# Performance work log

Measured on AMD Instinct MI355X. Metric: run time of the kernel, lower is better.

## Reference

```python
import jax, jax.numpy as jnp
import numpy as np

P = 5.0  # p-norm order from init_kwargs


def setup_inputs() -> dict:
    key = jax.random.key(0)
    k1, k2 = jax.random.split(key)
    B, N, M, C = 8, 4096, 4096, 3
    x = jax.random.normal(k1, (B, N, C), dtype=jnp.float32)
    y = jax.random.normal(k2, (B, M, C), dtype=jnp.float32)
    return {"x": x, "y": y}


def _pnorm(v, axis):
    # (sum |v|^p)^(1/p), matching torch.norm(p=5)
    return jnp.sum(jnp.abs(v) ** P, axis=axis) ** (1.0 / P)


def reference(x, y):
    # Squared Euclidean distance matrix [B, N, M]
    d = (-2.0 * jnp.einsum("bnc,bmc->bnm", x, y)
         + jnp.sum(x * x, -1)[:, :, None]
         + jnp.sum(y * y, -1)[:, None, :])
    idx1 = jnp.argmin(d, axis=2)  # [B, N]: nearest y for each x
    idx2 = jnp.argmin(d, axis=1)  # [B, M]: nearest x for each y
    nn_y = jnp.take_along_axis(y, idx1[..., None], axis=1)  # [B, N, 3]
    nn_x = jnp.take_along_axis(x, idx2[..., None], axis=1)  # [B, M, 3]
    pc1 = _pnorm(x - nn_y, axis=-1)  # [B, N]
    pc2 = _pnorm(y - nn_x, axis=-1)  # [B, M]
    result2 = _pnorm(pc1, axis=-1) + _pnorm(pc2, axis=-1)  # [B]
    return jnp.mean(result2)
```

## Files before the change

### kernel.cpp

```cpp
#include <hip/hip_runtime.h>
#include <math.h>


#define BQ      256
#define QPT     4
#define QP      (QPT / 2)
#define SPLITS  16
#define CH      256
#define GS      8
#define NG      (CH / GS)
#define BIGOFF  64.0f
#define NQTOT   65536
#define NTILE   64

typedef float f32x2 __attribute__((ext_vector_type(2)));

static __device__ __forceinline__ f32x2 mk2(float s) { f32x2 v; v.x = s; v.y = s; return v; }
static __device__ __forceinline__ f32x2 fma2(f32x2 a, f32x2 b, f32x2 c) {
    return __builtin_elementwise_fma(a, b, c);
}
static __device__ __forceinline__ f32x2 min2(f32x2 a, f32x2 b) {
    return __builtin_elementwise_min(a, b);
}
__device__ __forceinline__ unsigned int float_ord(float f) {
    unsigned int u = __float_as_uint(f);
    return (u & 0x80000000u) ? ~u : (u | 0x80000000u);
}

#define WS_ACC  0
#define WS_FCNT 64
#define WS_TAB  4096

__global__ __launch_bounds__(BQ) void chamfer_scan_r8(
    const float* __restrict__ x, const float* __restrict__ y,
    unsigned long long* __restrict__ tab, float* __restrict__ acc,
    unsigned int* __restrict__ fcnt)
{
    __shared__ float4 sref[CH];

    const int bid   = blockIdx.x;
    const int split = bid & (SPLITS - 1);
    const int tq    = bid >> 4;
    const int dir   = tq >> 5;
    const int b     = (tq >> 2) & 7;
    const int t4    = tq & 3;

    if (bid == 0 && threadIdx.x < 32) {
        if (threadIdx.x < 16) acc[threadIdx.x] = 0.0f;
        if (threadIdx.x == 16) *fcnt = 0u;
    }

    const float* Q; const float* R;
    if (dir == 0) { Q = x + (size_t)b * 4096 * 3; R = y + (size_t)b * 4096 * 3; }
    else          { Q = y + (size_t)b * 4096 * 3; R = x + (size_t)b * 4096 * 3; }

    const int tid = threadIdx.x;

    if (tid < CH / 2) {
        const float* rp = R + (size_t)(split * CH + 2 * tid) * 3;
        const float f0 = rp[0], f1 = rp[1], f2 = rp[2];
        const float f3 = rp[3], f4 = rp[4], f5 = rp[5];
        const float h0 = fmaf(0.5f * f0, f0, fmaf(0.5f * f1, f1, fmaf(0.5f * f2, f2, BIGOFF)));
        const float h1 = fmaf(0.5f * f3, f3, fmaf(0.5f * f4, f4, fmaf(0.5f * f5, f5, BIGOFF)));
        sref[2 * tid]     = make_float4(f0, f3, f1, f4);
        sref[2 * tid + 1] = make_float4(f2, f5, h0, h1);
    }

    f32x2 nqx[QP], nqy[QP], nqz[QP];
    #pragma unroll
    for (int p = 0; p < QP; ++p) {
        const int ql0 = t4 * 1024 + (2 * p) * 256 + tid;
        const int ql1 = ql0 + 256;
        nqx[p].x = -Q[ql0 * 3 + 0]; nqx[p].y = -Q[ql1 * 3 + 0];
        nqy[p].x = -Q[ql0 * 3 + 1]; nqy[p].y = -Q[ql1 * 3 + 1];
        nqz[p].x = -Q[ql0 * 3 + 2]; nqz[p].y = -Q[ql1 * 3 + 2];
    }
    __syncthreads();

    f32x2 best2[QP]; int bgA[QP], bgB[QP];
    #pragma unroll
    for (int p = 0; p < QP; ++p) { best2[p] = mk2(3.4e38f); bgA[p] = 0; bgB[p] = 0; }

    #pragma unroll 2
    for (int g = 0; g < NG; ++g) {
        f32x2 macc[QP];
        #pragma unroll
        for (int p = 0; p < QP; ++p) macc[p] = mk2(3.4e38f);
        #pragma unroll
        for (int k = 0; k < GS / 2; ++k) {
            const float4 a = sref[(g * 4 + k) * 2];
            const float4 c = sref[(g * 4 + k) * 2 + 1];
            const f32x2 rxl = mk2(a.x), rxh = mk2(a.y);
            const f32x2 ryl = mk2(a.z), ryh = mk2(a.w);
            const f32x2 rzl = mk2(c.x), rzh = mk2(c.y);
            const f32x2 hl  = mk2(c.z), hh2 = mk2(c.w);
            #pragma unroll
            for (int p = 0; p < QP; ++p) {
                const f32x2 tA = fma2(nqx[p], rxl, fma2(nqy[p], ryl, fma2(nqz[p], rzl, hl)));
                const f32x2 tB = fma2(nqx[p], rxh, fma2(nqy[p], ryh, fma2(nqz[p], rzh, hh2)));
                macc[p] = min2(macc[p], min2(tA, tB));
            }
        }
        #pragma unroll
        for (int p = 0; p < QP; ++p) {
            const bool cA = macc[p].x < best2[p].x;
            best2[p].x = cA ? macc[p].x : best2[p].x;
            bgA[p]     = cA ? g : bgA[p];
            const bool cB = macc[p].y < best2[p].y;
            best2[p].y = cB ? macc[p].y : best2[p].y;
            bgB[p]     = cB ? g : bgB[p];
        }
    }

    #pragma unroll
    for (int p = 0; p < QP; ++p) {
        #pragma unroll
        for (int hh = 0; hh < 2; ++hh) {
            const float bscore = hh ? best2[p].y : best2[p].x;
            const int   bg     = hh ? bgB[p]     : bgA[p];
            const float qx = hh ? -nqx[p].y : -nqx[p].x;
            const float qy = hh ? -nqy[p].y : -nqy[p].x;
            const float qz = hh ? -nqz[p].y : -nqz[p].x;
            const int basej = split * CH + bg * GS;
            int bj = basej;
            #pragma unroll
            for (int j = GS - 1; j >= 0; --j) {
                const float* rp = R + (size_t)(basej + j) * 3;
                const float rx = rp[0], ry = rp[1], rz = rp[2];
                const float h = fmaf(0.5f * rx, rx, fmaf(0.5f * ry, ry, fmaf(0.5f * rz, rz, BIGOFF)));
                const float s = fmaf(-qx, rx, fmaf(-qy, ry, fmaf(-qz, rz, h)));
                if (s == bscore) bj = basej + j;
            }
            const size_t qidx = (size_t)tq * 1024 + (2 * p + hh) * 256 + tid;
            const unsigned long long key =
                ~(((unsigned long long)__float_as_uint(bscore) << 32) | (unsigned int)bj);
            atomicMax(&tab[qidx], key);
        }
    }
}

__global__ __launch_bounds__(BQ) void chamfer_gather_fin_r8(
    const float* __restrict__ x, const float* __restrict__ y,
    const unsigned long long* __restrict__ tab,
    float* __restrict__ acc, unsigned int* __restrict__ fcnt,
    float* __restrict__ out)
{
    __shared__ float red[4];
    __shared__ int s_done;

    const int tid = threadIdx.x;
    const int gq  = blockIdx.x * BQ + tid;
    const int dir = gq >> 15;
    const int rem = gq & 32767;
    const int b   = rem >> 12;
    const int q   = rem & 4095;

    const float* Q; const float* R;
    if (dir == 0) { Q = x + (size_t)b * 4096 * 3; R = y + (size_t)b * 4096 * 3; }
    else          { Q = y + (size_t)b * 4096 * 3; R = x + (size_t)b * 4096 * 3; }

    const unsigned long long w = ~tab[gq];
    const int j = (int)(unsigned int)w;
    const float dx = Q[q * 3 + 0] - R[(size_t)j * 3 + 0];
    const float dy = Q[q * 3 + 1] - R[(size_t)j * 3 + 1];
    const float dz = Q[q * 3 + 2] - R[(size_t)j * 3 + 2];
    const float ax = fabsf(dx), ay = fabsf(dy), az = fabsf(dz);
    const float ax2 = ax * ax, ay2 = ay * ay, az2 = az * az;
    float s = ax2 * ax2 * ax + ay2 * ay2 * ay + az2 * az2 * az;

    #pragma unroll
    for (int off = 32; off > 0; off >>= 1) s += __shfl_down(s, off, 64);
    const int wid = tid >> 6, lane = tid & 63;
    if (lane == 0) red[wid] = s;
    __syncthreads();

    if (tid == 0) {
        atomicAdd(&acc[b * 2 + dir], red[0] + red[1] + red[2] + red[3]);
        __threadfence();
        const unsigned int done = atomicAdd(fcnt, 1u);
        s_done = (done == gridDim.x - 1);
    }
    __syncthreads();
    if (!s_done) return;

    __threadfence();
    if (tid < 64) {
        float v = 0.0f;
        if (tid < 16) {
            const float a = __hip_atomic_load(&acc[tid], __ATOMIC_RELAXED,
                                              __HIP_MEMORY_SCOPE_AGENT);
            v = exp2f(0.2f * log2f(a));
        }
        #pragma unroll
        for (int off = 8; off > 0; off >>= 1) v += __shfl_down(v, off, 64);
        if (tid == 0) out[0] = v * 0.125f;
    }
}

__global__ __launch_bounds__(BQ) void chamfer_nn_split_kernel(
    const float* __restrict__ x, const float* __restrict__ y,
    unsigned long long* __restrict__ packed, int N, int M)
{
    __shared__ float4 sref[1024];
    const int bid = blockIdx.x, split = bid & 3, qb = bid >> 2;
    const int tile = qb & 15, dir = (qb >> 4) & 1, b = qb >> 5;
    const float* Q; const float* R;
    if (dir == 0) { Q = x + (size_t)b * N * 3; R = y + (size_t)b * M * 3; }
    else          { Q = y + (size_t)b * M * 3; R = x + (size_t)b * N * 3; }
    const int tid = threadIdx.x, q = tile * BQ + tid, base = split * 1024;
    for (int j = tid; j < 1024; j += BQ) {
        const float rx = R[(size_t)(base + j) * 3 + 0];
        const float ry = R[(size_t)(base + j) * 3 + 1];
        const float rz = R[(size_t)(base + j) * 3 + 2];
        sref[j] = make_float4(rx, ry, rz, 0.5f * (rx * rx + ry * ry + rz * rz));
    }
    __syncthreads();
    const float qx = Q[q * 3 + 0], qy = Q[q * 3 + 1], qz = Q[q * 3 + 2];
    float best = 3.4e38f; int bestj = base;
    #pragma unroll 8
    for (int j = 0; j < 1024; ++j) {
        const float4 r = sref[j];
        float t = __fmaf_rn(-qx, r.x, r.w);
        t = __fmaf_rn(-qy, r.y, t);
        t = __fmaf_rn(-qz, r.z, t);
        const bool c = t < best;
        best = c ? t : best; bestj = c ? (base + j) : bestj;
    }
    const size_t idx = ((size_t)dir * 8 + b) * (size_t)N + q;
    atomicMin(&packed[idx], ((unsigned long long)float_ord(best) << 32) | (unsigned int)bestj);
}

__global__ __launch_bounds__(BQ) void chamfer_gather_kernel(
    const float* __restrict__ x, const float* __restrict__ y,
    const unsigned long long* __restrict__ packed,
    float* __restrict__ acc, int N, int M)
{
    __shared__ float red[4];
    const int tid = threadIdx.x;
    const size_t gq = (size_t)blockIdx.x * BQ + tid;
    const int dir = (int)(gq / ((size_t)8 * N));
    const size_t rem = gq - (size_t)dir * 8 * N;
    const int b = (int)(rem / N), q = (int)(rem - (size_t)b * N);
    const float* Q; const float* R;
    if (dir == 0) { Q = x + (size_t)b * N * 3; R = y + (size_t)b * M * 3; }
    else          { Q = y + (size_t)b * M * 3; R = x + (size_t)b * N * 3; }
    const int j = (int)(unsigned int)packed[gq];
    const float dx = Q[q * 3 + 0] - R[(size_t)j * 3 + 0];
    const float dy = Q[q * 3 + 1] - R[(size_t)j * 3 + 1];
    const float dz = Q[q * 3 + 2] - R[(size_t)j * 3 + 2];
    const float ax = fabsf(dx), ay = fabsf(dy), az = fabsf(dz);
    const float ax2 = ax * ax, ay2 = ay * ay, az2 = az * az;
    float s = ax2 * ax2 * ax + ay2 * ay2 * ay + az2 * az2 * az;
    #pragma unroll
    for (int off = 32; off > 0; off >>= 1) s += __shfl_down(s, off, 64);
    const int wid = tid >> 6, lane = tid & 63;
    if (lane == 0) red[wid] = s;
    __syncthreads();
    if (tid == 0) atomicAdd(&acc[b * 2 + dir], red[0] + red[1] + red[2] + red[3]);
}

__global__ void chamfer_finalize_kernel(const float* __restrict__ acc,
                                        float* __restrict__ out)
{
    if (threadIdx.x == 0 && blockIdx.x == 0) {
        float total = 0.0f;
        #pragma unroll
        for (int i = 0; i < 16; ++i) total += powf(acc[i], 0.2f);
        *out = total * 0.125f;
    }
}

extern "C" void kernel_launch(void* const* d_in, const int* in_sizes, int n_in,
                              void* d_out, int out_size, void* d_ws, size_t ws_size,
                              hipStream_t stream)
{
    const float* x = (const float*)d_in[0];
    const float* y = (const float*)d_in[1];
    float* out = (float*)d_out;
    const int N = in_sizes[0] / 24;
    const int M = in_sizes[1] / 24;

    const size_t needed = WS_TAB + (size_t)NQTOT * 8;

    if (N == 4096 && M == 4096 && ws_size >= needed) {
        unsigned char* ws = (unsigned char*)d_ws;
        float* acc = (float*)(ws + WS_ACC);
        unsigned int* fcnt = (unsigned int*)(ws + WS_FCNT);
        unsigned long long* tab = (unsigned long long*)(ws + WS_TAB);
        chamfer_scan_r8<<<NTILE * SPLITS, BQ, 0, stream>>>(x, y, tab, acc, fcnt);
        chamfer_gather_fin_r8<<<NQTOT / BQ, BQ, 0, stream>>>(x, y, tab, acc, fcnt, out);
    } else {
        unsigned char* ws = (unsigned char*)d_ws;
        float* acc = (float*)ws;
        unsigned long long* ptab = (unsigned long long*)(ws + 4096);
        const size_t nQ = (size_t)2 * 8 * N;
        hipMemsetAsync(acc, 0, 64, stream);
        hipMemsetAsync(ptab, 0xFF, nQ * 8, stream);
        chamfer_nn_split_kernel<<<(int)(nQ / BQ) * 4, BQ, 0, stream>>>(x, y, ptab, N, M);
        chamfer_gather_kernel<<<(int)(nQ / BQ), BQ, 0, stream>>>(x, y, ptab, acc, N, M);
        chamfer_finalize_kernel<<<1, 64, 0, stream>>>(acc, out);
    }
}
```

Before: 90.05 us.

## Fuse gather and finalize into the scan kernel via per-tile completion counters

Merges the two-kernel path into one. Each tile counts its finished split blocks with an atomic counter; the last block to finish a tile gathers the nearest neighbours, computes the p-norm partial sum and writes it to a per-tile slot. A global counter then picks the final block, which computes the result. This removes a kernel launch and the extra pass over the table. Counters are compared against a canary value read from the workspace and reset to it at the end, which assumes the workspace holds consistent values across calls.

```diff
diff --git a/kernel.cpp b/kernel.cpp
--- a/kernel.cpp
+++ b/kernel.cpp
@@ -27,16 +27,23 @@
     return (u & 0x80000000u) ? ~u : (u | 0x80000000u);
 }
 
-#define WS_ACC  0
-#define WS_FCNT 64
-#define WS_TAB  4096
-
-__global__ __launch_bounds__(BQ) void chamfer_scan_r8(
+#define WS_ACC    0
+#define WS_CANARY 128
+#define WS_GCNT   192
+#define WS_TCNT   256
+#define WS_PSUM   1024
+#define WS_TAB    4096
+
+__global__ __launch_bounds__(BQ) void chamfer_fused_r9(
     const float* __restrict__ x, const float* __restrict__ y,
-    unsigned long long* __restrict__ tab, float* __restrict__ acc,
-    unsigned int* __restrict__ fcnt)
+    unsigned long long* __restrict__ tab,
+    unsigned int* __restrict__ tcnt, unsigned int* __restrict__ gcnt,
+    const unsigned int* __restrict__ canary_p,
+    float* __restrict__ psum, float* __restrict__ out)
 {
     __shared__ float4 sref[CH];
+    __shared__ float red[4];
+    __shared__ int s_flag;
 
     const int bid   = blockIdx.x;
     const int split = bid & (SPLITS - 1);
@@ -45,10 +52,7 @@
     const int b     = (tq >> 2) & 7;
     const int t4    = tq & 3;
 
-    if (bid == 0 && threadIdx.x < 32) {
-        if (threadIdx.x < 16) acc[threadIdx.x] = 0.0f;
-        if (threadIdx.x == 16) *fcnt = 0u;
-    }
+    const unsigned int canary = *canary_p;
 
     const float* Q; const float* R;
     if (dir == 0) { Q = x + (size_t)b * 4096 * 3; R = y + (size_t)b * 4096 * 3; }
@@ -137,64 +141,68 @@
             atomicMax(&tab[qidx], key);
         }
     }
-}
-
-__global__ __launch_bounds__(BQ) void chamfer_gather_fin_r8(
-    const float* __restrict__ x, const float* __restrict__ y,
-    const unsigned long long* __restrict__ tab,
-    float* __restrict__ acc, unsigned int* __restrict__ fcnt,
-    float* __restrict__ out)
-{
-    __shared__ float red[4];
-    __shared__ int s_done;
-
-    const int tid = threadIdx.x;
-    const int gq  = blockIdx.x * BQ + tid;
-    const int dir = gq >> 15;
-    const int rem = gq & 32767;
-    const int b   = rem >> 12;
-    const int q   = rem & 4095;
-
-    const float* Q; const float* R;
-    if (dir == 0) { Q = x + (size_t)b * 4096 * 3; R = y + (size_t)b * 4096 * 3; }
-    else          { Q = y + (size_t)b * 4096 * 3; R = x + (size_t)b * 4096 * 3; }
-
-    const unsigned long long w = ~tab[gq];
-    const int j = (int)(unsigned int)w;
-    const float dx = Q[q * 3 + 0] - R[(size_t)j * 3 + 0];
-    const float dy = Q[q * 3 + 1] - R[(size_t)j * 3 + 1];
-    const float dz = Q[q * 3 + 2] - R[(size_t)j * 3 + 2];
-    const float ax = fabsf(dx), ay = fabsf(dy), az = fabsf(dz);
-    const float ax2 = ax * ax, ay2 = ay * ay, az2 = az * az;
-    float s = ax2 * ax2 * ax + ay2 * ay2 * ay + az2 * az2 * az;
-
-    #pragma unroll
-    for (int off = 32; off > 0; off >>= 1) s += __shfl_down(s, off, 64);
+
+    __threadfence();
+    __syncthreads();
+    if (tid == 0) {
+        const unsigned int old = atomicAdd(&tcnt[tq], 1u);
+        s_flag = (old == canary + (SPLITS - 1));
+    }
+    __syncthreads();
+    if (!s_flag) return;
+
+    __threadfence();
+    float sthr = 0.0f;
+    #pragma unroll
+    for (int k = 0; k < 4; ++k) {
+        const int gq = tq * 1024 + k * 256 + tid;
+        const int q  = t4 * 1024 + k * 256 + tid;
+        const unsigned long long w =
+            ~__hip_atomic_load(&tab[gq], __ATOMIC_RELAXED, __HIP_MEMORY_SCOPE_AGENT);
+        const int j = (int)(unsigned int)w;
+        const float dx = Q[q * 3 + 0] - R[(size_t)j * 3 + 0];
+        const float dy = Q[q * 3 + 1] - R[(size_t)j * 3 + 1];
+        const float dz = Q[q * 3 + 2] - R[(size_t)j * 3 + 2];
+        const float ax = fabsf(dx), ay = fabsf(dy), az = fabsf(dz);
+        const float ax2 = ax * ax, ay2 = ay * ay, az2 = az * az;
+        sthr += ax2 * ax2 * ax + ay2 * ay2 * ay + az2 * az2 * az;
+    }
+    #pragma unroll
+    for (int off = 32; off > 0; off >>= 1) sthr += __shfl_down(sthr, off, 64);
     const int wid = tid >> 6, lane = tid & 63;
-    if (lane == 0) red[wid] = s;
+    if (lane == 0) red[wid] = sthr;
     __syncthreads();
 
     if (tid == 0) {
-        atomicAdd(&acc[b * 2 + dir], red[0] + red[1] + red[2] + red[3]);
+        __hip_atomic_store(&psum[tq], red[0] + red[1] + red[2] + red[3],
+                           __ATOMIC_RELAXED, __HIP_MEMORY_SCOPE_AGENT);
         __threadfence();
-        const unsigned int done = atomicAdd(fcnt, 1u);
-        s_done = (done == gridDim.x - 1);
-    }
-    __syncthreads();
-    if (!s_done) return;
+        const unsigned int old = atomicAdd(gcnt, 1u);
+        s_flag = (old == canary + (NTILE - 1));
+    }
+    __syncthreads();
+    if (!s_flag) return;
 
     __threadfence();
     if (tid < 64) {
         float v = 0.0f;
         if (tid < 16) {
-            const float a = __hip_atomic_load(&acc[tid], __ATOMIC_RELAXED,
-                                              __HIP_MEMORY_SCOPE_AGENT);
+            const int fb = tid >> 1, fdir = tid & 1;
+            float a = 0.0f;
+            #pragma unroll
+            for (int t = 0; t < 4; ++t)
+                a += __hip_atomic_load(&psum[fdir * 32 + fb * 4 + t],
+                                       __ATOMIC_RELAXED, __HIP_MEMORY_SCOPE_AGENT);
             v = exp2f(0.2f * log2f(a));
         }
         #pragma unroll
         for (int off = 8; off > 0; off >>= 1) v += __shfl_down(v, off, 64);
         if (tid == 0) out[0] = v * 0.125f;
     }
+    if (tid < 64)
+        __hip_atomic_store(&tcnt[tid], canary, __ATOMIC_RELAXED, __HIP_MEMORY_SCOPE_AGENT);
+    if (tid == 0)
+        __hip_atomic_store(gcnt, canary, __ATOMIC_RELAXED, __HIP_MEMORY_SCOPE_AGENT);
 }
 
 __global__ __launch_bounds__(BQ) void chamfer_nn_split_kernel(
@@ -284,11 +292,13 @@
 
     if (N == 4096 && M == 4096 && ws_size >= needed) {
         unsigned char* ws = (unsigned char*)d_ws;
-        float* acc = (float*)(ws + WS_ACC);
-        unsigned int* fcnt = (unsigned int*)(ws + WS_FCNT);
         unsigned long long* tab = (unsigned long long*)(ws + WS_TAB);
-        chamfer_scan_r8<<<NTILE * SPLITS, BQ, 0, stream>>>(x, y, tab, acc, fcnt);
-        chamfer_gather_fin_r8<<<NQTOT / BQ, BQ, 0, stream>>>(x, y, tab, acc, fcnt, out);
+        unsigned int* tcnt = (unsigned int*)(ws + WS_TCNT);
+        unsigned int* gcnt = (unsigned int*)(ws + WS_GCNT);
+        const unsigned int* canary = (const unsigned int*)(ws + WS_CANARY);
+        float* psum = (float*)(ws + WS_PSUM);
+        chamfer_fused_r9<<<NTILE * SPLITS, BQ, 0, stream>>>(
+            x, y, tab, tcnt, gcnt, canary, psum, out);
     } else {
         unsigned char* ws = (unsigned char*)d_ws;
         float* acc = (float*)ws;
```

Measured after the change: 156.1 us. 73.3% more time.
